# Kernel optimization log

Hardware: AMD Instinct MI355X
Metric: run time of the kernel (lower is better)

Reference implementation:

```python
import jax, jax.numpy as jnp
import numpy as np

B, I, S = 1024, 128, 512
UNFOLDS = 6


def setup_inputs() -> dict:
    key = jax.random.key(0)
    ks = jax.random.split(key, 16)
    inputs = jax.random.normal(ks[0], (B, I), dtype=jnp.float32)
    hx = jax.random.normal(ks[1], (B, S), dtype=jnp.float32)
    # learned parameters, initialized per _get_variables()
    input_w = jnp.ones((I,), dtype=jnp.float32)
    input_b = jnp.zeros((I,), dtype=jnp.float32)
    sensory_mu = jax.random.uniform(ks[2], (I, S)) * 0.5 + 0.3
    sensory_sigma = jax.random.uniform(ks[3], (I, S)) * 5.0 + 3.0
    sensory_W = jax.random.uniform(ks[4], (I, S), minval=0.01, maxval=1.0)
    sensory_erev = (2.0 * jax.random.randint(ks[5], (I, S), 0, 2) - 1.0).astype(jnp.float32)
    mu = jax.random.uniform(ks[6], (S, S)) * 0.5 + 0.3
    sigma = jax.random.uniform(ks[7], (S, S)) * 5.0 + 3.0
    W = jax.random.uniform(ks[8], (S, S), minval=0.01, maxval=1.0)
    erev = (2.0 * jax.random.randint(ks[9], (S, S), 0, 2) - 1.0).astype(jnp.float32)
    vleak = jax.random.uniform(ks[10], (S,)) * 0.4 - 0.2
    gleak = jnp.ones((S,), dtype=jnp.float32)   # gleak_init_min == gleak_init_max == 1
    cm_t = jnp.full((S,), 0.5, dtype=jnp.float32)  # cm_init_min == cm_init_max == 0.5
    return dict(inputs=inputs, hx=hx, input_w=input_w, input_b=input_b,
                sensory_mu=sensory_mu, sensory_sigma=sensory_sigma,
                sensory_W=sensory_W, sensory_erev=sensory_erev,
                mu=mu, sigma=sigma, W=W, erev=erev,
                vleak=vleak, gleak=gleak, cm_t=cm_t)


def reference(inputs, hx, input_w, input_b, sensory_mu, sensory_sigma,
              sensory_W, sensory_erev, mu, sigma, W, erev, vleak, gleak, cm_t):
    # Affine input mapping
    x = inputs * input_w + input_b                      # [B, I]
    # Sensory synapse activation (computed once): [B, I, S]
    sens_act = sensory_W * jax.nn.sigmoid(sensory_sigma * (x[:, :, None] - sensory_mu))
    w_num_sensory = jnp.sum(sens_act * sensory_erev, axis=1)  # [B, S]
    w_den_sensory = jnp.sum(sens_act, axis=1)                 # [B, S]

    v = hx
    for _ in range(UNFOLDS):
        # Recurrent synapse activation: broadcast state over presynaptic dim -> [B, S, S]
        w_act = W * jax.nn.sigmoid(sigma * (v[:, :, None] - mu))
        w_num = jnp.sum(w_act * erev, axis=1) + w_num_sensory   # [B, S]
        w_den = jnp.sum(w_act, axis=1) + w_den_sensory          # [B, S]
        numerator = cm_t * v + gleak * vleak + w_num
        denominator = cm_t + gleak + w_den
        v = numerator / denominator
    # forward returns (outputs, next_state), which are the same tensor
    return v
```

## Files before the change

kernel.cpp:

```cpp
#include <hip/hip_runtime.h>
#include <math.h>


#define B_TOT 1024
#define I_DIM 128
#define S_DIM 512
#define UNFOLDS 6
#define L2E 1.4426950408889634f

typedef float v2f __attribute__((ext_vector_type(2)));

#define OFF_RECQ 0
#define OFF_VA   (OFF_RECQ + S_DIM * S_DIM * 4)
#define OFF_SN   (OFF_VA + S_DIM * B_TOT)
#define OFF_SD   (OFF_SN + S_DIM * B_TOT)
#define OFF_SENQ (OFF_SD + S_DIM * B_TOT)
#define OFF_XT   (OFF_SENQ + S_DIM * I_DIM * 4)
#define OFF_VB   OFF_SENQ

__global__ __launch_bounds__(256) void prep_all(
    const float* __restrict__ inputs, const float* __restrict__ hx,
    const float* __restrict__ input_w, const float* __restrict__ input_b,
    const float* __restrict__ s_mu, const float* __restrict__ s_sigma,
    const float* __restrict__ s_W, const float* __restrict__ s_erev,
    const float* __restrict__ mu, const float* __restrict__ sigma,
    const float* __restrict__ W, const float* __restrict__ erev,
    float* __restrict__ ws)
{
    __shared__ float tA[32][33], tB[32][33], tC[32][33];
    const int bid = blockIdx.x;
    const int tx = threadIdx.x & 31, ty = threadIdx.x >> 5;

    if (bid < 320) {
        bool rec = bid < 256;
        int b2  = rec ? bid : bid - 256;
        int tri = b2 >> 4;
        int tcj = b2 & 15;
        const float* sgp = rec ? sigma : s_sigma;
        const float* mup = rec ? mu    : s_mu;
        const float* wp  = rec ? W     : s_W;
        const float* erp = rec ? erev  : s_erev;
        #pragma unroll
        for (int rr = 0; rr < 4; ++rr) {
            int r = ty + rr * 8;
            int idx = (tri * 32 + r) * S_DIM + tcj * 32 + tx;
            float sg = sgp[idx], m = mup[idx], w = wp[idx], er = erp[idx];
            tA[r][tx] = -sg * L2E;
            tB[r][tx] = sg * m * L2E;
            tC[r][tx] = w * er;
        }
        __syncthreads();
        float4* dst = (float4*)(ws + (rec ? OFF_RECQ : OFF_SENQ));
        int ld = rec ? S_DIM : I_DIM;
        #pragma unroll
        for (int rr = 0; rr < 4; ++rr) {
            int jj = ty + rr * 8;
            float wn = tC[tx][jj];
            dst[(tcj * 32 + jj) * ld + tri * 32 + tx] =
                make_float4(tA[tx][jj], tB[tx][jj], wn, fabsf(wn));
        }
    } else if (bid < 448) {
        int b2 = bid - 320;
        int tbr = b2 >> 2, tci = b2 & 3;
        int i = tci * 32 + tx;
        float wi = input_w[i], bi = input_b[i];
        #pragma unroll
        for (int rr = 0; rr < 4; ++rr) {
            int r = ty + rr * 8;
            tA[r][tx] = inputs[(tbr * 32 + r) * I_DIM + i] * wi + bi;
        }
        __syncthreads();
        float* xT = ws + OFF_XT;
        #pragma unroll
        for (int rr = 0; rr < 4; ++rr) {
            int ii = ty + rr * 8;
            xT[(tci * 32 + ii) * B_TOT + tbr * 32 + tx] = tA[tx][ii];
        }
    } else {
        int b2 = bid - 448;
        int tbr = b2 >> 4, tcj = b2 & 15;
        #pragma unroll
        for (int rr = 0; rr < 4; ++rr) {
            int r = ty + rr * 8;
            tA[r][tx] = hx[(tbr * 32 + r) * S_DIM + tcj * 32 + tx];
        }
        __syncthreads();
        float* vA = ws + OFF_VA;
        #pragma unroll
        for (int rr = 0; rr < 4; ++rr) {
            int jj = ty + rr * 8;
            vA[(tcj * 32 + jj) * B_TOT + tbr * 32 + tx] = tA[tx][jj];
        }
    }
}

__device__ __forceinline__ void sig_step(v2f ac, v2f ww, v2f v, v2f one,
                                         v2f& n, v2f& d)
{
    v2f t;
    asm("v_pk_fma_f32 %0, %1, %2, %1 op_sel:[0,0,1] op_sel_hi:[0,1,1]"
        : "=v"(t) : "v"(ac), "v"(v));
    float e0, e1;
    asm("v_exp_f32 %0, %1" : "=v"(e0) : "v"(t.x));
    asm("v_exp_f32 %0, %1" : "=v"(e1) : "v"(t.y));
    v2f e; e.x = e0; e.y = e1;
    v2f r;
    asm("v_pk_add_f32 %0, %1, %2" : "=v"(r) : "v"(e), "v"(one));
    float s0, s1;
    asm("v_rcp_f32 %0, %1" : "=v"(s0) : "v"(r.x));
    asm("v_rcp_f32 %0, %1" : "=v"(s1) : "v"(r.y));
    v2f s; s.x = s0; s.y = s1;
    asm("v_pk_fma_f32 %0, %1, %2, %0 op_sel:[0,0,0] op_sel_hi:[0,1,1]"
        : "+v"(n) : "v"(ww), "v"(s));
    asm("v_pk_fma_f32 %0, %1, %2, %0 op_sel:[1,0,0] op_sel_hi:[1,1,1]"
        : "+v"(d) : "v"(ww), "v"(s));
}

__device__ __forceinline__ void col_reduce_pk(
    const float4* __restrict__ qp,
    const float* __restrict__ vsrc,
    int nd, int tb, v2f one, v2f& n, v2f& d)
{
    #pragma unroll 8
    for (int i = 0; i < nd; ++i) {
        float4 q = qp[i];
        v2f ac; ac.x = q.x; ac.y = q.y;
        v2f ww; ww.x = q.z; ww.y = q.w;
        v2f v = *(const v2f*)(vsrc + (size_t)i * B_TOT + tb);
        sig_step(ac, ww, v, one, n, d);
    }
}

__global__ __launch_bounds__(512, 4) void sensory_kernel(float* __restrict__ ws)
{
    const int j = blockIdx.x;
    const int tb = threadIdx.x * 2;
    v2f one; one.x = 1.0f; one.y = 1.0f;
    v2f n; n.x = 0.f; n.y = 0.f;
    v2f d; d.x = 0.f; d.y = 0.f;
    col_reduce_pk((const float4*)(ws + OFF_SENQ) + j * I_DIM,
                  ws + OFF_XT, I_DIM, tb, one, n, d);
    *(v2f*)&ws[OFF_SN + j * B_TOT + tb] = n;
    *(v2f*)&ws[OFF_SD + j * B_TOT + tb] = d;
}

__global__ __launch_bounds__(512, 4) void unfold_kernel(
    const float* __restrict__ ws, const float* __restrict__ vsrc,
    float* __restrict__ vdst,
    const float* __restrict__ gleak, const float* __restrict__ vleak,
    const float* __restrict__ cm_t,
    float* __restrict__ out, int write_out)
{
    const int j = blockIdx.x;
    const int tb = threadIdx.x * 2;
    v2f one; one.x = 1.0f; one.y = 1.0f;
    v2f n = *(const v2f*)&ws[OFF_SN + j * B_TOT + tb];
    v2f d = *(const v2f*)&ws[OFF_SD + j * B_TOT + tb];
    col_reduce_pk((const float4*)(ws + OFF_RECQ) + j * S_DIM,
                  vsrc, S_DIM, tb, one, n, d);

    v2f vo = *(const v2f*)&vsrc[j * B_TOT + tb];
    float gl = gleak[j], vl = vleak[j], cm = cm_t[j];
    float glvl = gl * vl, cg = cm + gl;

    float r0 = (fmaf(cm, vo.x, glvl) + n.x) / (cg + d.x);
    float r1 = (fmaf(cm, vo.y, glvl) + n.y) / (cg + d.y);

    if (write_out) {
        out[tb * S_DIM + j] = r0;
        out[(tb + 1) * S_DIM + j] = r1;
    } else {
        v2f rr; rr.x = r0; rr.y = r1;
        *(v2f*)&vdst[j * B_TOT + tb] = rr;
    }
}

extern "C" void kernel_launch(void* const* d_in, const int* in_sizes, int n_in,
                              void* d_out, int out_size, void* d_ws, size_t ws_size,
                              hipStream_t stream) {
    const float* inputs   = (const float*)d_in[0];
    const float* hx       = (const float*)d_in[1];
    const float* input_w  = (const float*)d_in[2];
    const float* input_b  = (const float*)d_in[3];
    const float* s_mu     = (const float*)d_in[4];
    const float* s_sigma  = (const float*)d_in[5];
    const float* s_W      = (const float*)d_in[6];
    const float* s_erev   = (const float*)d_in[7];
    const float* mu       = (const float*)d_in[8];
    const float* sigma    = (const float*)d_in[9];
    const float* W        = (const float*)d_in[10];
    const float* erev     = (const float*)d_in[11];
    const float* vleak    = (const float*)d_in[12];
    const float* gleak    = (const float*)d_in[13];
    const float* cm_t     = (const float*)d_in[14];
    float* out = (float*)d_out;
    float* ws  = (float*)d_ws;

    prep_all<<<960, 256, 0, stream>>>(inputs, hx, input_w, input_b,
                                      s_mu, s_sigma, s_W, s_erev,
                                      mu, sigma, W, erev, ws);

    sensory_kernel<<<S_DIM, 512, 0, stream>>>(ws);

    float* vA = ws + OFF_VA;
    float* vB = ws + OFF_VB;
    for (int u = 0; u < UNFOLDS; ++u) {
        const float* src = (u & 1) ? vB : vA;
        float* dst       = (u & 1) ? vA : vB;
        int last = (u == UNFOLDS - 1);
        unfold_kernel<<<S_DIM, 512, 0, stream>>>(
            ws, src, dst, gleak, vleak, cm_t, out, last);
    }
}
```

Measured before the change: 434.4 us.

## Replace sigmoid exp/rcp with fp16 LDS lookup table and linear interpolation

Replaces the transcendental exp plus reciprocal sigmoid in the inner reduction with a 1024-entry lookup table held in shared memory. Each entry stores a half2 of value and slope, and the result comes from a single fma_mix interpolation. The table is replicated 16 times with per-lane offsets to reduce LDS bank conflicts. Inputs are clamped to ±14 in the exp2 domain, so the sigmoid is approximated with fp16 table precision. This adds a table build and a 64KB LDS allocation per block, which lowers occupancy.

```diff
diff --git a/kernel.cpp b/kernel.cpp
--- a/kernel.cpp
+++ b/kernel.cpp
@@ -1,4 +1,5 @@
 #include <hip/hip_runtime.h>
+#include <hip/hip_fp16.h>
 #include <math.h>
 
 
@@ -7,8 +8,9 @@
 #define S_DIM 512
 #define UNFOLDS 6
 #define L2E 1.4426950408889634f
-
-typedef float v2f __attribute__((ext_vector_type(2)));
+#define TBL_N 1024
+#define NREP 16
+#define T_MAX 14.0f
 
 #define OFF_RECQ 0
 #define OFF_VA   (OFF_RECQ + S_DIM * S_DIM * 4)
@@ -17,6 +19,14 @@
 #define OFF_SENQ (OFF_SD + S_DIM * B_TOT)
 #define OFF_XT   (OFF_SENQ + S_DIM * I_DIM * 4)
 #define OFF_VB   OFF_SENQ
+
+__device__ __forceinline__ float ffract(float x) {
+#if __has_builtin(__builtin_amdgcn_fractf)
+    return __builtin_amdgcn_fractf(x);
+#else
+    return x - floorf(x);
+#endif
+}
 
 __global__ __launch_bounds__(256) void prep_all(
     const float* __restrict__ inputs, const float* __restrict__ hx,
@@ -30,6 +40,8 @@
     __shared__ float tA[32][33], tB[32][33], tC[32][33];
     const int bid = blockIdx.x;
     const int tx = threadIdx.x & 31, ty = threadIdx.x >> 5;
+    const float SCALE = (float)TBL_N / (2.0f * T_MAX);
+    const float OFF   = (float)(TBL_N / 2);
 
     if (bid < 320) {
         bool rec = bid < 256;
@@ -45,8 +57,8 @@
             int r = ty + rr * 8;
             int idx = (tri * 32 + r) * S_DIM + tcj * 32 + tx;
             float sg = sgp[idx], m = mup[idx], w = wp[idx], er = erp[idx];
-            tA[r][tx] = -sg * L2E;
-            tB[r][tx] = sg * m * L2E;
+            tA[r][tx] = -sg * L2E * SCALE;
+            tB[r][tx] = sg * m * L2E * SCALE + OFF;
             tC[r][tx] = w * er;
         }
         __syncthreads();
@@ -94,54 +106,67 @@
     }
 }
 
-__device__ __forceinline__ void sig_step(v2f ac, v2f ww, v2f v, v2f one,
-                                         v2f& n, v2f& d)
-{
-    v2f t;
-    asm("v_pk_fma_f32 %0, %1, %2, %1 op_sel:[0,0,1] op_sel_hi:[0,1,1]"
-        : "=v"(t) : "v"(ac), "v"(v));
-    float e0, e1;
-    asm("v_exp_f32 %0, %1" : "=v"(e0) : "v"(t.x));
-    asm("v_exp_f32 %0, %1" : "=v"(e1) : "v"(t.y));
-    v2f e; e.x = e0; e.y = e1;
-    v2f r;
-    asm("v_pk_add_f32 %0, %1, %2" : "=v"(r) : "v"(e), "v"(one));
-    float s0, s1;
-    asm("v_rcp_f32 %0, %1" : "=v"(s0) : "v"(r.x));
-    asm("v_rcp_f32 %0, %1" : "=v"(s1) : "v"(r.y));
-    v2f s; s.x = s0; s.y = s1;
-    asm("v_pk_fma_f32 %0, %1, %2, %0 op_sel:[0,0,0] op_sel_hi:[0,1,1]"
-        : "+v"(n) : "v"(ww), "v"(s));
-    asm("v_pk_fma_f32 %0, %1, %2, %0 op_sel:[1,0,0] op_sel_hi:[1,1,1]"
-        : "+v"(d) : "v"(ww), "v"(s));
-}
-
-__device__ __forceinline__ void col_reduce_pk(
+__device__ __forceinline__ void build_tbl(unsigned* tbl, int tid)
+{
+    const float hb = (2.0f * T_MAX) / (float)TBL_N;
+    for (int k = tid; k < TBL_N; k += 512) {
+        float t0 = (float)(k - TBL_N / 2) * hb;
+        float s0 = 1.0f / (1.0f + exp2f(t0));
+        float s1 = 1.0f / (1.0f + exp2f(t0 + hb));
+        __half2 h = __floats2half2_rn(s0, s1 - s0);
+        unsigned e = __builtin_bit_cast(unsigned, h);
+        #pragma unroll
+        for (int r = 0; r < NREP; ++r)
+            tbl[k * NREP + ((tid + r) & (NREP - 1))] = e;
+    }
+}
+
+__device__ __forceinline__ void sig_elem(float A, float C, float Wn, float Wp,
+                                         float v, const char* tbase, float CLHI,
+                                         float& n, float& d)
+{
+    float f = fmaf(A, v, C);
+    f = __builtin_amdgcn_fmed3f(f, 0.0f, CLHI);
+    unsigned k = (unsigned)f;
+    float fr = ffract(f);
+    unsigned hv = *(const unsigned*)(tbase + (k << 6));
+    float s;
+    asm("v_fma_mix_f32 %0, %1, %2, %1 op_sel:[1,0,0] op_sel_hi:[1,0,1]"
+        : "=v"(s) : "v"(hv), "v"(fr));
+    n = fmaf(Wn, s, n);
+    d = fmaf(Wp, s, d);
+}
+
+__device__ __forceinline__ void col_reduce_tbl(
     const float4* __restrict__ qp,
     const float* __restrict__ vsrc,
-    int nd, int tb, v2f one, v2f& n, v2f& d)
+    int nd, int tb, const char* tbase, float CLHI,
+    float& n0, float& n1, float& d0, float& d1)
 {
     #pragma unroll 8
     for (int i = 0; i < nd; ++i) {
         float4 q = qp[i];
-        v2f ac; ac.x = q.x; ac.y = q.y;
-        v2f ww; ww.x = q.z; ww.y = q.w;
-        v2f v = *(const v2f*)(vsrc + (size_t)i * B_TOT + tb);
-        sig_step(ac, ww, v, one, n, d);
+        float2 v = *(const float2*)(vsrc + (size_t)i * B_TOT + tb);
+        sig_elem(q.x, q.y, q.z, q.w, v.x, tbase, CLHI, n0, d0);
+        sig_elem(q.x, q.y, q.z, q.w, v.y, tbase, CLHI, n1, d1);
     }
 }
 
 __global__ __launch_bounds__(512, 4) void sensory_kernel(float* __restrict__ ws)
 {
+    __shared__ unsigned tbl[TBL_N * NREP];
+    const int tid = threadIdx.x;
     const int j = blockIdx.x;
-    const int tb = threadIdx.x * 2;
-    v2f one; one.x = 1.0f; one.y = 1.0f;
-    v2f n; n.x = 0.f; n.y = 0.f;
-    v2f d; d.x = 0.f; d.y = 0.f;
-    col_reduce_pk((const float4*)(ws + OFF_SENQ) + j * I_DIM,
-                  ws + OFF_XT, I_DIM, tb, one, n, d);
-    *(v2f*)&ws[OFF_SN + j * B_TOT + tb] = n;
-    *(v2f*)&ws[OFF_SD + j * B_TOT + tb] = d;
+    const int tb = tid * 2;
+    build_tbl(tbl, tid);
+    __syncthreads();
+    const char* tbase = (const char*)tbl + ((tid & (NREP - 1)) << 2);
+    const float CLHI = (float)(TBL_N - 1);
+    float n0 = 0.f, n1 = 0.f, d0 = 0.f, d1 = 0.f;
+    col_reduce_tbl((const float4*)(ws + OFF_SENQ) + j * I_DIM,
+                   ws + OFF_XT, I_DIM, tb, tbase, CLHI, n0, n1, d0, d1);
+    *(float2*)&ws[OFF_SN + j * B_TOT + tb] = make_float2(n0, n1);
+    *(float2*)&ws[OFF_SD + j * B_TOT + tb] = make_float2(d0, d1);
 }
 
 __global__ __launch_bounds__(512, 4) void unfold_kernel(
@@ -151,27 +176,33 @@
     const float* __restrict__ cm_t,
     float* __restrict__ out, int write_out)
 {
+    __shared__ unsigned tbl[TBL_N * NREP];
+    const int tid = threadIdx.x;
     const int j = blockIdx.x;
-    const int tb = threadIdx.x * 2;
-    v2f one; one.x = 1.0f; one.y = 1.0f;
-    v2f n = *(const v2f*)&ws[OFF_SN + j * B_TOT + tb];
-    v2f d = *(const v2f*)&ws[OFF_SD + j * B_TOT + tb];
-    col_reduce_pk((const float4*)(ws + OFF_RECQ) + j * S_DIM,
-                  vsrc, S_DIM, tb, one, n, d);
-
-    v2f vo = *(const v2f*)&vsrc[j * B_TOT + tb];
+    const int tb = tid * 2;
+    build_tbl(tbl, tid);
+    __syncthreads();
+    const char* tbase = (const char*)tbl + ((tid & (NREP - 1)) << 2);
+    const float CLHI = (float)(TBL_N - 1);
+
+    float2 sn = *(const float2*)&ws[OFF_SN + j * B_TOT + tb];
+    float2 sd = *(const float2*)&ws[OFF_SD + j * B_TOT + tb];
+    float n0 = sn.x, n1 = sn.y, d0 = sd.x, d1 = sd.y;
+    col_reduce_tbl((const float4*)(ws + OFF_RECQ) + j * S_DIM,
+                   vsrc, S_DIM, tb, tbase, CLHI, n0, n1, d0, d1);
+
+    float2 vo = *(const float2*)&vsrc[j * B_TOT + tb];
     float gl = gleak[j], vl = vleak[j], cm = cm_t[j];
     float glvl = gl * vl, cg = cm + gl;
 
-    float r0 = (fmaf(cm, vo.x, glvl) + n.x) / (cg + d.x);
-    float r1 = (fmaf(cm, vo.y, glvl) + n.y) / (cg + d.y);
+    float r0 = (fmaf(cm, vo.x, glvl) + n0) / (cg + d0);
+    float r1 = (fmaf(cm, vo.y, glvl) + n1) / (cg + d1);
 
     if (write_out) {
         out[tb * S_DIM + j] = r0;
         out[(tb + 1) * S_DIM + j] = r1;
     } else {
-        v2f rr; rr.x = r0; rr.y = r1;
-        *(v2f*)&vdst[j * B_TOT + tb] = rr;
+        *(float2*)&vdst[j * B_TOT + tb] = make_float2(r0, r1);
     }
 }
 
```

Result: no change. 432.5 us (-0.4%).

## Compute sigmoid in packed fp16 with polynomial exp2 and bit-trick reciprocal

Applied to the files above, without the earlier changes.

Stores the precomputed synapse parameters, inputs and the state vector in fp16, halving their memory traffic. It replaces the transcendental v_exp/v_rcp sigmoid with a packed-half routine: clamping, an exp2 built from a cubic polynomial plus exponent bit assembly, and a magic-constant reciprocal refined by one Newton step. Accumulation stays in fp32 through fma_mix. This is meant to avoid the quarter-rate transcendental units and process two lanes per instruction, but it adds approximation error in sigmoid and in the fp16 state that carries across unfolds.

```diff
diff --git a/kernel.cpp b/kernel.cpp
--- a/kernel.cpp
+++ b/kernel.cpp
@@ -1,4 +1,5 @@
 #include <hip/hip_runtime.h>
+#include <hip/hip_fp16.h>
 #include <math.h>
 
 
@@ -8,15 +9,85 @@
 #define UNFOLDS 6
 #define L2E 1.4426950408889634f
 
-typedef float v2f __attribute__((ext_vector_type(2)));
-
-#define OFF_RECQ 0
-#define OFF_VA   (OFF_RECQ + S_DIM * S_DIM * 4)
-#define OFF_SN   (OFF_VA + S_DIM * B_TOT)
-#define OFF_SD   (OFF_SN + S_DIM * B_TOT)
-#define OFF_SENQ (OFF_SD + S_DIM * B_TOT)
-#define OFF_XT   (OFF_SENQ + S_DIM * I_DIM * 4)
-#define OFF_VB   OFF_SENQ
+#define BY_RECH 0u
+#define BY_SENH (BY_RECH + 2097152u)
+#define BY_XH   (BY_SENH + 524288u)
+#define BY_VA   (BY_XH + 262144u)
+#define BY_VB   (BY_VA + 1048576u)
+#define BY_SN   (BY_VB + 1048576u)
+#define BY_SD   (BY_SN + 2097152u)
+
+struct Cst { unsigned kLO, kHI, k1536, c3, c2, c1, one2, m2, magic, c26097, sh10; };
+
+__device__ __forceinline__ unsigned hpak(float x) {
+    __half h = __float2half_rn(x);
+    unsigned short b = __builtin_bit_cast(unsigned short, h);
+    return ((unsigned)b << 16) | (unsigned)b;
+}
+
+__device__ __forceinline__ Cst mkc() {
+    Cst c;
+    c.kLO    = hpak(-14.0f);
+    c.kHI    = hpak(13.5f);
+    c.k1536  = hpak(1536.0f);
+    c.c3     = hpak(0.05550411f);
+    c.c2     = hpak(0.24022651f);
+    c.c1     = hpak(0.69314718f);
+    c.one2   = hpak(1.0f);
+    c.m2     = hpak(-2.0f);
+    c.magic  = 0x77987798u;
+    c.c26097 = (26097u << 16) | 26097u;
+    c.sh10   = (10u << 16) | 10u;
+    return c;
+}
+
+__device__ __forceinline__ void sigpair(unsigned AC, unsigned WW, unsigned vp,
+                                        const Cst& C,
+                                        float& n0, float& n1, float& d0, float& d1)
+{
+    unsigned t, z, kf, f, p, scb, sc, e, d, y, q, sn;
+    asm("v_pk_fma_f16 %0, %1, %2, %1 op_sel:[0,0,1] op_sel_hi:[0,1,1]"
+        : "=v"(t) : "s"(AC), "v"(vp));
+    asm("v_pk_max_f16 %0, %0, %1" : "+v"(t) : "v"(C.kLO));
+    asm("v_pk_min_f16 %0, %0, %1" : "+v"(t) : "v"(C.kHI));
+    asm("v_pk_add_f16 %0, %1, %2" : "=v"(z) : "v"(t), "v"(C.k1536));
+    asm("v_pk_add_f16 %0, %1, %2 neg_lo:[0,1] neg_hi:[0,1]"
+        : "=v"(kf) : "v"(z), "v"(C.k1536));
+    asm("v_pk_add_f16 %0, %1, %2 neg_lo:[0,1] neg_hi:[0,1]"
+        : "=v"(f) : "v"(t), "v"(kf));
+    asm("v_pk_fma_f16 %0, %1, %2, %3" : "=v"(p) : "v"(C.c3), "v"(f), "v"(C.c2));
+    asm("v_pk_fma_f16 %0, %0, %1, %2" : "+v"(p) : "v"(f), "v"(C.c1));
+    asm("v_pk_fma_f16 %0, %0, %1, %2" : "+v"(p) : "v"(f), "v"(C.one2));
+    asm("v_pk_sub_u16 %0, %1, %2" : "=v"(scb) : "v"(z), "v"(C.c26097));
+    asm("v_pk_lshlrev_b16 %0, %1, %2" : "=v"(sc) : "v"(C.sh10), "v"(scb));
+    asm("v_pk_mul_f16 %0, %1, %2" : "=v"(e) : "v"(p), "v"(sc));
+    asm("v_pk_add_f16 %0, %1, %2" : "=v"(d) : "v"(e), "v"(C.one2));
+    asm("v_pk_sub_u16 %0, %1, %2" : "=v"(y) : "v"(C.magic), "v"(d));
+    asm("v_pk_fma_f16 %0, %1, %2, %3" : "=v"(q) : "v"(d), "v"(y), "v"(C.m2));
+    asm("v_pk_mul_f16 %0, %1, %2" : "=v"(sn) : "v"(y), "v"(q));
+    asm("v_fma_mix_f32 %0, %1, %2, %0 op_sel:[0,0,0] op_sel_hi:[1,1,0]"
+        : "+v"(n0) : "s"(WW), "v"(sn));
+    asm("v_fma_mix_f32 %0, %1, %2, %0 op_sel:[0,1,0] op_sel_hi:[1,1,0]"
+        : "+v"(n1) : "s"(WW), "v"(sn));
+    asm("v_fma_mix_f32 %0, %1, %2, %0 op_sel:[1,0,0] op_sel_hi:[1,1,0]"
+        : "+v"(d0) : "s"(WW), "v"(sn));
+    asm("v_fma_mix_f32 %0, %1, %2, %0 op_sel:[1,1,0] op_sel_hi:[1,1,0]"
+        : "+v"(d1) : "s"(WW), "v"(sn));
+}
+
+__device__ __forceinline__ void reduce_f16(
+    const uint2* __restrict__ qp,
+    const unsigned* __restrict__ vrow,
+    int nd, int tid, const Cst& C,
+    float& n0, float& n1, float& d0, float& d1)
+{
+    #pragma unroll 4
+    for (int i = 0; i < nd; ++i) {
+        uint2 Q = qp[i];
+        unsigned vp = vrow[(size_t)i * (B_TOT / 2) + tid];
+        sigpair(Q.x, Q.y, vp, C, n0, n1, d0, d1);
+    }
+}
 
 __global__ __launch_bounds__(256) void prep_all(
     const float* __restrict__ inputs, const float* __restrict__ hx,
@@ -25,7 +96,7 @@
     const float* __restrict__ s_W, const float* __restrict__ s_erev,
     const float* __restrict__ mu, const float* __restrict__ sigma,
     const float* __restrict__ W, const float* __restrict__ erev,
-    float* __restrict__ ws)
+    char* __restrict__ ws)
 {
     __shared__ float tA[32][33], tB[32][33], tC[32][33];
     const int bid = blockIdx.x;
@@ -50,14 +121,17 @@
             tC[r][tx] = w * er;
         }
         __syncthreads();
-        float4* dst = (float4*)(ws + (rec ? OFF_RECQ : OFF_SENQ));
+        uint2* dst = (uint2*)(ws + (rec ? BY_RECH : BY_SENH));
         int ld = rec ? S_DIM : I_DIM;
         #pragma unroll
         for (int rr = 0; rr < 4; ++rr) {
             int jj = ty + rr * 8;
-            float wn = tC[tx][jj];
-            dst[(tcj * 32 + jj) * ld + tri * 32 + tx] =
-                make_float4(tA[tx][jj], tB[tx][jj], wn, fabsf(wn));
+            float A = tA[tx][jj], Cc = tB[tx][jj], wn = tC[tx][jj];
+            __half2 ac = __floats2half2_rn(A, Cc);
+            __half2 ww = __floats2half2_rn(-wn, -fabsf(wn));
+            dst[(size_t)(tcj * 32 + jj) * ld + tri * 32 + tx] =
+                make_uint2(__builtin_bit_cast(unsigned, ac),
+                           __builtin_bit_cast(unsigned, ww));
         }
     } else if (bid < 448) {
         int b2 = bid - 320;
@@ -70,11 +144,12 @@
             tA[r][tx] = inputs[(tbr * 32 + r) * I_DIM + i] * wi + bi;
         }
         __syncthreads();
-        float* xT = ws + OFF_XT;
+        __half* xh = (__half*)(ws + BY_XH);
         #pragma unroll
         for (int rr = 0; rr < 4; ++rr) {
             int ii = ty + rr * 8;
-            xT[(tci * 32 + ii) * B_TOT + tbr * 32 + tx] = tA[tx][ii];
+            xh[(size_t)(tci * 32 + ii) * B_TOT + tbr * 32 + tx] =
+                __float2half_rn(tA[tx][ii]);
         }
     } else {
         int b2 = bid - 448;
@@ -85,93 +160,62 @@
             tA[r][tx] = hx[(tbr * 32 + r) * S_DIM + tcj * 32 + tx];
         }
         __syncthreads();
-        float* vA = ws + OFF_VA;
+        __half* va = (__half*)(ws + BY_VA);
         #pragma unroll
         for (int rr = 0; rr < 4; ++rr) {
             int jj = ty + rr * 8;
-            vA[(tcj * 32 + jj) * B_TOT + tbr * 32 + tx] = tA[tx][jj];
-        }
-    }
-}
-
-__device__ __forceinline__ void sig_step(v2f ac, v2f ww, v2f v, v2f one,
-                                         v2f& n, v2f& d)
-{
-    v2f t;
-    asm("v_pk_fma_f32 %0, %1, %2, %1 op_sel:[0,0,1] op_sel_hi:[0,1,1]"
-        : "=v"(t) : "v"(ac), "v"(v));
-    float e0, e1;
-    asm("v_exp_f32 %0, %1" : "=v"(e0) : "v"(t.x));
-    asm("v_exp_f32 %0, %1" : "=v"(e1) : "v"(t.y));
-    v2f e; e.x = e0; e.y = e1;
-    v2f r;
-    asm("v_pk_add_f32 %0, %1, %2" : "=v"(r) : "v"(e), "v"(one));
-    float s0, s1;
-    asm("v_rcp_f32 %0, %1" : "=v"(s0) : "v"(r.x));
-    asm("v_rcp_f32 %0, %1" : "=v"(s1) : "v"(r.y));
-    v2f s; s.x = s0; s.y = s1;
-    asm("v_pk_fma_f32 %0, %1, %2, %0 op_sel:[0,0,0] op_sel_hi:[0,1,1]"
-        : "+v"(n) : "v"(ww), "v"(s));
-    asm("v_pk_fma_f32 %0, %1, %2, %0 op_sel:[1,0,0] op_sel_hi:[1,1,1]"
-        : "+v"(d) : "v"(ww), "v"(s));
-}
-
-__device__ __forceinline__ void col_reduce_pk(
-    const float4* __restrict__ qp,
-    const float* __restrict__ vsrc,
-    int nd, int tb, v2f one, v2f& n, v2f& d)
-{
-    #pragma unroll 8
-    for (int i = 0; i < nd; ++i) {
-        float4 q = qp[i];
-        v2f ac; ac.x = q.x; ac.y = q.y;
-        v2f ww; ww.x = q.z; ww.y = q.w;
-        v2f v = *(const v2f*)(vsrc + (size_t)i * B_TOT + tb);
-        sig_step(ac, ww, v, one, n, d);
-    }
-}
-
-__global__ __launch_bounds__(512, 4) void sensory_kernel(float* __restrict__ ws)
-{
-    const int j = blockIdx.x;
-    const int tb = threadIdx.x * 2;
-    v2f one; one.x = 1.0f; one.y = 1.0f;
-    v2f n; n.x = 0.f; n.y = 0.f;
-    v2f d; d.x = 0.f; d.y = 0.f;
-    col_reduce_pk((const float4*)(ws + OFF_SENQ) + j * I_DIM,
-                  ws + OFF_XT, I_DIM, tb, one, n, d);
-    *(v2f*)&ws[OFF_SN + j * B_TOT + tb] = n;
-    *(v2f*)&ws[OFF_SD + j * B_TOT + tb] = d;
-}
-
-__global__ __launch_bounds__(512, 4) void unfold_kernel(
-    const float* __restrict__ ws, const float* __restrict__ vsrc,
-    float* __restrict__ vdst,
+            va[(size_t)(tcj * 32 + jj) * B_TOT + tbr * 32 + tx] =
+                __float2half_rn(tA[tx][jj]);
+        }
+    }
+}
+
+__global__ __launch_bounds__(512, 4) void sensory_f16(char* __restrict__ ws)
+{
+    const int j = blockIdx.x, tid = threadIdx.x, tb = tid * 2;
+    Cst C = mkc();
+    const uint2* qp = (const uint2*)(ws + BY_SENH) + (size_t)j * I_DIM;
+    const unsigned* xrow = (const unsigned*)(ws + BY_XH);
+    float n0 = 0.f, n1 = 0.f, d0 = 0.f, d1 = 0.f;
+    reduce_f16(qp, xrow, I_DIM, tid, C, n0, n1, d0, d1);
+    float* SN = (float*)(ws + BY_SN);
+    float* SD = (float*)(ws + BY_SD);
+    *(float2*)&SN[(size_t)j * B_TOT + tb] = make_float2(n0, n1);
+    *(float2*)&SD[(size_t)j * B_TOT + tb] = make_float2(d0, d1);
+}
+
+__global__ __launch_bounds__(512, 4) void unfold_f16(
+    const char* __restrict__ ws, const unsigned* __restrict__ vsrc,
+    unsigned* __restrict__ vdst,
     const float* __restrict__ gleak, const float* __restrict__ vleak,
     const float* __restrict__ cm_t,
     float* __restrict__ out, int write_out)
 {
-    const int j = blockIdx.x;
-    const int tb = threadIdx.x * 2;
-    v2f one; one.x = 1.0f; one.y = 1.0f;
-    v2f n = *(const v2f*)&ws[OFF_SN + j * B_TOT + tb];
-    v2f d = *(const v2f*)&ws[OFF_SD + j * B_TOT + tb];
-    col_reduce_pk((const float4*)(ws + OFF_RECQ) + j * S_DIM,
-                  vsrc, S_DIM, tb, one, n, d);
-
-    v2f vo = *(const v2f*)&vsrc[j * B_TOT + tb];
+    const int j = blockIdx.x, tid = threadIdx.x, tb = tid * 2;
+    Cst C = mkc();
+    const uint2* qp = (const uint2*)(ws + BY_RECH) + (size_t)j * S_DIM;
+    const float* SN = (const float*)(ws + BY_SN);
+    const float* SD = (const float*)(ws + BY_SD);
+    float2 sn2 = *(const float2*)&SN[(size_t)j * B_TOT + tb];
+    float2 sd2 = *(const float2*)&SD[(size_t)j * B_TOT + tb];
+    float n0 = sn2.x, n1 = sn2.y, d0 = sd2.x, d1 = sd2.y;
+    reduce_f16(qp, vsrc, S_DIM, tid, C, n0, n1, d0, d1);
+
+    unsigned vop = vsrc[(size_t)j * (B_TOT / 2) + tid];
+    __half2 voh = __builtin_bit_cast(__half2, vop);
+    float vo0 = __half2float(voh.x), vo1 = __half2float(voh.y);
     float gl = gleak[j], vl = vleak[j], cm = cm_t[j];
     float glvl = gl * vl, cg = cm + gl;
 
-    float r0 = (fmaf(cm, vo.x, glvl) + n.x) / (cg + d.x);
-    float r1 = (fmaf(cm, vo.y, glvl) + n.y) / (cg + d.y);
+    float r0 = (fmaf(cm, vo0, glvl) + n0) / (cg + d0);
+    float r1 = (fmaf(cm, vo1, glvl) + n1) / (cg + d1);
 
     if (write_out) {
         out[tb * S_DIM + j] = r0;
         out[(tb + 1) * S_DIM + j] = r1;
     } else {
-        v2f rr; rr.x = r0; rr.y = r1;
-        *(v2f*)&vdst[j * B_TOT + tb] = rr;
+        vdst[(size_t)j * (B_TOT / 2) + tid] =
+            __builtin_bit_cast(unsigned, __floats2half2_rn(r0, r1));
     }
 }
 
@@ -194,21 +238,21 @@
     const float* gleak    = (const float*)d_in[13];
     const float* cm_t     = (const float*)d_in[14];
     float* out = (float*)d_out;
-    float* ws  = (float*)d_ws;
+    char* ws   = (char*)d_ws;
 
     prep_all<<<960, 256, 0, stream>>>(inputs, hx, input_w, input_b,
                                       s_mu, s_sigma, s_W, s_erev,
                                       mu, sigma, W, erev, ws);
 
-    sensory_kernel<<<S_DIM, 512, 0, stream>>>(ws);
-
-    float* vA = ws + OFF_VA;
-    float* vB = ws + OFF_VB;
+    sensory_f16<<<S_DIM, 512, 0, stream>>>(ws);
+
+    unsigned* vA = (unsigned*)(ws + BY_VA);
+    unsigned* vB = (unsigned*)(ws + BY_VB);
     for (int u = 0; u < UNFOLDS; ++u) {
-        const float* src = (u & 1) ? vB : vA;
-        float* dst       = (u & 1) ? vA : vB;
+        const unsigned* src = (u & 1) ? vB : vA;
+        unsigned* dst       = (u & 1) ? vA : vB;
         int last = (u == UNFOLDS - 1);
-        unfold_kernel<<<S_DIM, 512, 0, stream>>>(
+        unfold_f16<<<S_DIM, 512, 0, stream>>>(
             ws, src, dst, gleak, vleak, cm_t, out, last);
     }
 }
```

Measured after the change: 571.3 us. 1.32x slower.
